# Kernel tuning notes

Measured on AMD Instinct MI355X. Metric: run time of the kernel, lower is better.

The kernel has to match this reference:

```python
import jax, jax.numpy as jnp
import numpy as np

B = 16          # batch (num decode sequences)
H = 16          # num heads (== num kv heads)
D = 128         # head dim
BLOCK = 16      # tokens per cache block
BPS = 128       # blocks per sequence
NB = B * BPS    # total cache blocks = 2048
S = BPS * BLOCK # max context len per seq = 2048
SCALE = 0.08838834764831845  # 1/sqrt(128)


def setup_inputs() -> dict:
    key = jax.random.key(0)
    ks = jax.random.split(key, 5)
    q = jax.random.normal(ks[0], (B, H, D), dtype=jnp.float32)
    k = jax.random.normal(ks[1], (B, H, D), dtype=jnp.float32)
    v = jax.random.normal(ks[2], (B, H, D), dtype=jnp.float32)
    k_cache = jax.random.normal(ks[3], (NB, BLOCK, H, D), dtype=jnp.float32)
    v_cache = jax.random.normal(ks[4], (NB, BLOCK, H, D), dtype=jnp.float32)
    # identity paged layout: seq i owns blocks [i*BPS, (i+1)*BPS)
    block_tables = jnp.arange(NB, dtype=jnp.int32).reshape(B, BPS)
    # new token goes into the last slot of each sequence's last block
    slot_mapping = (jnp.arange(B, dtype=jnp.int32) * BPS + (BPS - 1)) * BLOCK + (BLOCK - 1)
    context_lens = jnp.full((B,), S, dtype=jnp.int32)
    return {"q": q, "k": k, "v": v, "k_cache": k_cache, "v_cache": v_cache,
            "block_tables": block_tables, "slot_mapping": slot_mapping,
            "context_lens": context_lens}


def reference(q, k, v, k_cache, v_cache, block_tables, slot_mapping, context_lens):
    nb, block_size, h, d = k_cache.shape
    b = q.shape[0]
    # --- store_kvcache: scatter new K/V token into flat cache (all slots valid) ---
    flat_k = k_cache.reshape(nb * block_size, h, d).at[slot_mapping].set(k)
    flat_v = v_cache.reshape(nb * block_size, h, d).at[slot_mapping].set(v)
    kc = flat_k.reshape(nb, block_size, h, d)
    vc = flat_v.reshape(nb, block_size, h, d)
    # --- paged gather: [B, BPS, BLOCK, H, D] -> [B, S, H, D] ---
    k_seq = kc[block_tables].reshape(b, -1, h, d)
    v_seq = vc[block_tables].reshape(b, -1, h, d)
    s = k_seq.shape[1]
    # --- masked single-token attention (q_len = 1) ---
    scores = jnp.einsum('bhd,bshd->bhs', q, k_seq) * SCALE
    mask = jnp.arange(s, dtype=jnp.int32)[None, :] < context_lens[:, None]  # [B, S]
    scores = jnp.where(mask[:, None, :], scores, -jnp.inf)
    p = jax.nn.softmax(scores, axis=-1)
    o = jnp.einsum('bhs,bshd->bhd', p, v_seq)  # [B, H, D]
    return o
```

## Files before the change

### kernel.cpp

```cpp
#include <hip/hip_runtime.h>
#include <math.h>

#define BB   16
#define HH   16
#define DD   128
#define BLK  16
#define BPS  128
#define SS   2048
#define SCALE_F 0.08838834764831845f

#define SPLIT 8
#define CHUNK (SS / SPLIT)
#define NT1   256
#define NW1   4
#define TPW1  (CHUNK / NW1)

__global__ __launch_bounds__(NT1, 8)
void pd_partial(const float* __restrict__ q,
                const float* __restrict__ knew,
                const float* __restrict__ vnew,
                const float* __restrict__ kc,
                const float* __restrict__ vc,
                const int*   __restrict__ bt,
                const int*   __restrict__ smap_g,
                const int*   __restrict__ clen,
                float*       __restrict__ ml,
                float*       __restrict__ pacc)
{
    __shared__ float sc[CHUNK];
    __shared__ int   rb[CHUNK];
    __shared__ float part[NW1][DD];
    __shared__ int   smap[BB];
    __shared__ float redm[NW1], reds[NW1];

    const int bid  = blockIdx.x;
    const int c    = bid & (SPLIT - 1);
    const int bh   = bid >> 3;
    const int b    = bh >> 4;
    const int h    = bh & 15;
    const int t    = threadIdx.x;
    const int lane = t & 63;
    const int wave = t >> 6;
    const int len  = clen[b];
    const int sbase = c * CHUNK;

    if (t < BB) smap[t] = smap_g[t];
    __syncthreads();

    {
        int s    = sbase + t;
        int pb   = bt[b * BPS + (s >> 4)];
        int slot = pb * BLK + (s & 15);
        int enc  = (slot * HH + h) * DD;
        #pragma unroll
        for (int j = 0; j < BB; ++j)
            if (slot == smap[j]) enc = -(j + 1);
        rb[t] = enc;
    }
    __syncthreads();

    const int half = lane >> 5;
    const int d4   = lane & 31;
    const float4 q4 = *(const float4*)(q + bh * DD + d4 * 4);
    const int w0 = wave * TPW1;

    #pragma unroll 8
    for (int i = 0; i < TPW1 / 2; ++i) {
        int sl  = w0 + i * 2 + half;
        int s   = sbase + sl;
        int enc = rb[sl];
        const float* kp = (enc >= 0)
            ? (kc + enc + d4 * 4)
            : (knew + ((-enc - 1) * HH + h) * DD + d4 * 4);
        float4 kv = *(const float4*)kp;
        float dot = q4.x * kv.x + q4.y * kv.y + q4.z * kv.z + q4.w * kv.w;
        dot += __shfl_xor(dot, 1);
        dot += __shfl_xor(dot, 2);
        dot += __shfl_xor(dot, 4);
        dot += __shfl_xor(dot, 8);
        dot += __shfl_xor(dot, 16);
        if (d4 == 0) sc[sl] = (s < len) ? dot * SCALE_F : -1e30f;
    }
    __syncthreads();

    float m = sc[t];
    #pragma unroll
    for (int msk = 32; msk >= 1; msk >>= 1)
        m = fmaxf(m, __shfl_xor(m, msk));
    if (lane == 0) redm[wave] = m;
    __syncthreads();
    const float M = fmaxf(fmaxf(redm[0], redm[1]), fmaxf(redm[2], redm[3]));

    float e = expf(sc[t] - M);
    sc[t] = e;
    float ssum = e;
    #pragma unroll
    for (int msk = 32; msk >= 1; msk >>= 1)
        ssum += __shfl_xor(ssum, msk);
    if (lane == 0) reds[wave] = ssum;
    __syncthreads();

    float4 acc = make_float4(0.f, 0.f, 0.f, 0.f);
    #pragma unroll 8
    for (int i = 0; i < TPW1 / 2; ++i) {
        int sl  = w0 + i * 2 + half;
        float p = sc[sl];
        int enc = rb[sl];
        const float* vp = (enc >= 0)
            ? (vc + enc + d4 * 4)
            : (vnew + ((-enc - 1) * HH + h) * DD + d4 * 4);
        float4 vv = *(const float4*)vp;
        acc.x += p * vv.x;
        acc.y += p * vv.y;
        acc.z += p * vv.z;
        acc.w += p * vv.w;
    }
    acc.x += __shfl_xor(acc.x, 32);
    acc.y += __shfl_xor(acc.y, 32);
    acc.z += __shfl_xor(acc.z, 32);
    acc.w += __shfl_xor(acc.w, 32);
    if (lane < 32) *(float4*)&part[wave][d4 * 4] = acc;
    __syncthreads();

    if (t < DD) {
        float o = part[0][t] + part[1][t] + part[2][t] + part[3][t];
        pacc[bid * DD + t] = o;
    }
    if (t == 0) {
        float L = reds[0] + reds[1] + reds[2] + reds[3];
        ml[bid * 2]     = M;
        ml[bid * 2 + 1] = L;
    }
}

__global__ __launch_bounds__(DD)
void pd_combine(const float* __restrict__ ml,
                const float* __restrict__ pacc,
                float*       __restrict__ out)
{
    const int bh = blockIdx.x;
    const int t  = threadIdx.x;

    float m[SPLIT], l[SPLIT];
    float M = -1e30f;
    #pragma unroll
    for (int i = 0; i < SPLIT; ++i) {
        m[i] = ml[(bh * SPLIT + i) * 2];
        l[i] = ml[(bh * SPLIT + i) * 2 + 1];
        M = fmaxf(M, m[i]);
    }
    float denom = 0.f, o = 0.f;
    #pragma unroll
    for (int i = 0; i < SPLIT; ++i) {
        float w = expf(m[i] - M);
        denom += w * l[i];
        o     += w * pacc[(bh * SPLIT + i) * DD + t];
    }
    out[bh * DD + t] = o / denom;
}

extern "C" void kernel_launch(void* const* d_in, const int* in_sizes, int n_in,
                              void* d_out, int out_size, void* d_ws, size_t ws_size,
                              hipStream_t stream)
{
    const float* q    = (const float*)d_in[0];
    const float* knew = (const float*)d_in[1];
    const float* vnew = (const float*)d_in[2];
    const float* kc   = (const float*)d_in[3];
    const float* vc   = (const float*)d_in[4];
    const int*   bt   = (const int*)d_in[5];
    const int*   smap = (const int*)d_in[6];
    const int*   clen = (const int*)d_in[7];
    float*       out  = (float*)d_out;

    float* ml   = (float*)d_ws;
    float* pacc = (float*)d_ws + BB * HH * SPLIT * 2;

    pd_partial<<<dim3(BB * HH * SPLIT), dim3(NT1), 0, stream>>>(
        q, knew, vnew, kc, vc, bt, smap, clen, ml, pacc);
    pd_combine<<<dim3(BB * HH), dim3(DD), 0, stream>>>(ml, pacc, out);
}
```

Baseline: 98.84 us.

## Process all heads per block with contiguous token rows and finer sequence split

```diff
diff --git a/kernel.cpp b/kernel.cpp
--- a/kernel.cpp
+++ b/kernel.cpp
@@ -9,13 +9,13 @@
 #define SS   2048
 #define SCALE_F 0.08838834764831845f
 
-#define SPLIT 8
-#define CHUNK (SS / SPLIT)
-#define NT1   256
-#define NW1   4
-#define TPW1  (CHUNK / NW1)
+#define SPLIT 32
+#define CHK   (SS / SPLIT)
+#define NT1   512
+#define NW1   8
+#define TPW   (CHK / NW1)
 
-__global__ __launch_bounds__(NT1, 8)
+__global__ __launch_bounds__(NT1, 2)
 void pd_partial(const float* __restrict__ q,
                 const float* __restrict__ knew,
                 const float* __restrict__ vnew,
@@ -27,109 +27,128 @@
                 float*       __restrict__ ml,
                 float*       __restrict__ pacc)
 {
-    __shared__ float sc[CHUNK];
-    __shared__ int   rb[CHUNK];
-    __shared__ float part[NW1][DD];
+    __shared__ float red[4 * 2048];
+    __shared__ float sc[HH * CHK];
+    __shared__ int   rbs[CHK];
     __shared__ int   smap[BB];
-    __shared__ float redm[NW1], reds[NW1];
 
     const int bid  = blockIdx.x;
     const int c    = bid & (SPLIT - 1);
-    const int bh   = bid >> 3;
-    const int b    = bh >> 4;
-    const int h    = bh & 15;
+    const int b    = bid >> 5;
     const int t    = threadIdx.x;
     const int lane = t & 63;
-    const int wave = t >> 6;
+    const int w    = t >> 6;
+    const int hh   = lane >> 5;
+    const int d4   = lane & 31;
     const int len  = clen[b];
-    const int sbase = c * CHUNK;
+    const int sbase = c * CHK;
 
     if (t < BB) smap[t] = smap_g[t];
     __syncthreads();
 
-    {
+    if (t < CHK) {
         int s    = sbase + t;
         int pb   = bt[b * BPS + (s >> 4)];
         int slot = pb * BLK + (s & 15);
-        int enc  = (slot * HH + h) * DD;
+        int enc  = slot * (HH * DD);
         #pragma unroll
         for (int j = 0; j < BB; ++j)
             if (slot == smap[j]) enc = -(j + 1);
-        rb[t] = enc;
+        rbs[t] = enc;
     }
     __syncthreads();
 
-    const int half = lane >> 5;
-    const int d4   = lane & 31;
-    const float4 q4 = *(const float4*)(q + bh * DD + d4 * 4);
-    const int w0 = wave * TPW1;
+    float4 qf[8];
+    #pragma unroll
+    for (int p = 0; p < 8; ++p)
+        qf[p] = *(const float4*)(q + b * (HH * DD) + (2 * p + hh) * DD + d4 * 4);
 
-    #pragma unroll 8
-    for (int i = 0; i < TPW1 / 2; ++i) {
-        int sl  = w0 + i * 2 + half;
-        int s   = sbase + sl;
-        int enc = rb[sl];
-        const float* kp = (enc >= 0)
-            ? (kc + enc + d4 * 4)
-            : (knew + ((-enc - 1) * HH + h) * DD + d4 * 4);
-        float4 kv = *(const float4*)kp;
-        float dot = q4.x * kv.x + q4.y * kv.y + q4.z * kv.z + q4.w * kv.w;
-        dot += __shfl_xor(dot, 1);
-        dot += __shfl_xor(dot, 2);
-        dot += __shfl_xor(dot, 4);
-        dot += __shfl_xor(dot, 8);
-        dot += __shfl_xor(dot, 16);
-        if (d4 == 0) sc[sl] = (s < len) ? dot * SCALE_F : -1e30f;
+    #pragma unroll
+    for (int i = 0; i < TPW; ++i) {
+        int tok = w + NW1 * i;
+        int enc = rbs[tok];
+        const float* rp = (enc >= 0) ? (kc + enc) : (knew + (-enc - 1) * (HH * DD));
+        #pragma unroll
+        for (int p = 0; p < 8; ++p) {
+            float4 kv = *(const float4*)(rp + p * 256 + lane * 4);
+            float d = qf[p].x * kv.x + qf[p].y * kv.y + qf[p].z * kv.z + qf[p].w * kv.w;
+            d += __shfl_xor(d, 1);
+            d += __shfl_xor(d, 2);
+            d += __shfl_xor(d, 4);
+            d += __shfl_xor(d, 8);
+            d += __shfl_xor(d, 16);
+            if (d4 == 0) sc[(2 * p + hh) * CHK + tok] = d * SCALE_F;
+        }
     }
     __syncthreads();
 
-    float m = sc[t];
-    #pragma unroll
-    for (int msk = 32; msk >= 1; msk >>= 1)
-        m = fmaxf(m, __shfl_xor(m, msk));
-    if (lane == 0) redm[wave] = m;
-    __syncthreads();
-    const float M = fmaxf(fmaxf(redm[0], redm[1]), fmaxf(redm[2], redm[3]));
-
-    float e = expf(sc[t] - M);
-    sc[t] = e;
-    float ssum = e;
-    #pragma unroll
-    for (int msk = 32; msk >= 1; msk >>= 1)
-        ssum += __shfl_xor(ssum, msk);
-    if (lane == 0) reds[wave] = ssum;
+    {
+        int h = 2 * w + hh;
+        int t0 = d4, t1 = d4 + 32;
+        float v0 = (sbase + t0 < len) ? sc[h * CHK + t0] : -1e30f;
+        float v1 = (sbase + t1 < len) ? sc[h * CHK + t1] : -1e30f;
+        float m = fmaxf(v0, v1);
+        #pragma unroll
+        for (int msk = 16; msk >= 1; msk >>= 1)
+            m = fmaxf(m, __shfl_xor(m, msk));
+        float e0 = expf(v0 - m), e1 = expf(v1 - m);
+        float sum = e0 + e1;
+        #pragma unroll
+        for (int msk = 16; msk >= 1; msk >>= 1)
+            sum += __shfl_xor(sum, msk);
+        sc[h * CHK + t0] = e0;
+        sc[h * CHK + t1] = e1;
+        if (d4 == 0) {
+            ml[((b * HH + h) * SPLIT + c) * 2]     = m;
+            ml[((b * HH + h) * SPLIT + c) * 2 + 1] = sum;
+        }
+    }
     __syncthreads();
 
-    float4 acc = make_float4(0.f, 0.f, 0.f, 0.f);
-    #pragma unroll 8
-    for (int i = 0; i < TPW1 / 2; ++i) {
-        int sl  = w0 + i * 2 + half;
-        float p = sc[sl];
-        int enc = rb[sl];
-        const float* vp = (enc >= 0)
-            ? (vc + enc + d4 * 4)
-            : (vnew + ((-enc - 1) * HH + h) * DD + d4 * 4);
-        float4 vv = *(const float4*)vp;
-        acc.x += p * vv.x;
-        acc.y += p * vv.y;
-        acc.z += p * vv.z;
-        acc.w += p * vv.w;
+    float4 acc[8];
+    #pragma unroll
+    for (int p = 0; p < 8; ++p) acc[p] = make_float4(0.f, 0.f, 0.f, 0.f);
+
+    #pragma unroll
+    for (int i = 0; i < TPW; ++i) {
+        int tok = w + NW1 * i;
+        int enc = rbs[tok];
+        const float* rp = (enc >= 0) ? (vc + enc) : (vnew + (-enc - 1) * (HH * DD));
+        #pragma unroll
+        for (int p = 0; p < 8; ++p) {
+            float4 vv = *(const float4*)(rp + p * 256 + lane * 4);
+            float pr = sc[(2 * p + hh) * CHK + tok];
+            acc[p].x += pr * vv.x;
+            acc[p].y += pr * vv.y;
+            acc[p].z += pr * vv.z;
+            acc[p].w += pr * vv.w;
+        }
     }
-    acc.x += __shfl_xor(acc.x, 32);
-    acc.y += __shfl_xor(acc.y, 32);
-    acc.z += __shfl_xor(acc.z, 32);
-    acc.w += __shfl_xor(acc.w, 32);
-    if (lane < 32) *(float4*)&part[wave][d4 * 4] = acc;
-    __syncthreads();
 
-    if (t < DD) {
-        float o = part[0][t] + part[1][t] + part[2][t] + part[3][t];
-        pacc[bid * DD + t] = o;
+    #pragma unroll
+    for (int r = 4; r >= 1; r >>= 1) {
+        if (w >= r && w < 2 * r) {
+            #pragma unroll
+            for (int p = 0; p < 8; ++p)
+                *(float4*)&red[(w - r) * 2048 + p * 256 + lane * 4] = acc[p];
+        }
+        __syncthreads();
+        if (w < r) {
+            #pragma unroll
+            for (int p = 0; p < 8; ++p) {
+                float4 o = *(const float4*)&red[w * 2048 + p * 256 + lane * 4];
+                acc[p].x += o.x; acc[p].y += o.y; acc[p].z += o.z; acc[p].w += o.w;
+            }
+        }
+        __syncthreads();
     }
-    if (t == 0) {
-        float L = reds[0] + reds[1] + reds[2] + reds[3];
-        ml[bid * 2]     = M;
-        ml[bid * 2 + 1] = L;
+
+    if (w == 0) {
+        #pragma unroll
+        for (int p = 0; p < 8; ++p) {
+            int h = 2 * p + hh;
+            *(float4*)&pacc[((b * HH + h) * SPLIT + c) * DD + d4 * 4] = acc[p];
+        }
     }
 }
 
@@ -141,22 +160,19 @@
     const int bh = blockIdx.x;
     const int t  = threadIdx.x;
 
-    float m[SPLIT], l[SPLIT];
-    float M = -1e30f;
-    #pragma unroll
+    float M = -1e30f, den = 0.f, o = 0.f;
+    #pragma unroll 8
     for (int i = 0; i < SPLIT; ++i) {
-        m[i] = ml[(bh * SPLIT + i) * 2];
-        l[i] = ml[(bh * SPLIT + i) * 2 + 1];
-        M = fmaxf(M, m[i]);
+        float mi = ml[(bh * SPLIT + i) * 2];
+        float li = ml[(bh * SPLIT + i) * 2 + 1];
+        float nm = fmaxf(M, mi);
+        float sOld = expf(M - nm);
+        float sNew = expf(mi - nm);
+        o   = o * sOld + sNew * pacc[(bh * SPLIT + i) * DD + t];
+        den = den * sOld + sNew * li;
+        M = nm;
     }
-    float denom = 0.f, o = 0.f;
-    #pragma unroll
-    for (int i = 0; i < SPLIT; ++i) {
-        float w = expf(m[i] - M);
-        denom += w * l[i];
-        o     += w * pacc[(bh * SPLIT + i) * DD + t];
-    }
-    out[bh * DD + t] = o / denom;
+    out[bh * DD + t] = o / den;
 }
 
 extern "C" void kernel_launch(void* const* d_in, const int* in_sizes, int n_in,
@@ -176,7 +192,7 @@
     float* ml   = (float*)d_ws;
     float* pacc = (float*)d_ws + BB * HH * SPLIT * 2;
 
-    pd_partial<<<dim3(BB * HH * SPLIT), dim3(NT1), 0, stream>>>(
+    pd_partial<<<dim3(BB * SPLIT), dim3(NT1), 0, stream>>>(
         q, knew, vnew, kc, vc, bt, smap, clen, ml, pacc);
     pd_combine<<<dim3(BB * HH), dim3(DD), 0, stream>>>(ml, pacc, out);
 }
```

Result: slower. 110.8 us (+12.1%).
